# Optimization experiments

Measured on AMD Instinct MI355X. Metric: run time of the kernel, lower is better.

The kernel has to match this reference:

```python
import jax, jax.numpy as jnp
import numpy as np

B, L1, L2 = 4, 2048, 2048
INP1_DIM = INP2_DIM = 1024
QK_DIM = V_DIM = 1024
HEAD_N = 16
QK_HEAD = QK_DIM // HEAD_N  # 64
V_HEAD = V_DIM // HEAD_N    # 64
SCALE = 1.0 / (QK_HEAD ** 0.5)


def _linear_params(key, out_dim, in_dim):
    # torch nn.Linear default init: U(-1/sqrt(in), 1/sqrt(in)) for W and b
    kw, kb = jax.random.split(key)
    bound = 1.0 / np.sqrt(in_dim)
    W = jax.random.uniform(kw, (out_dim, in_dim), jnp.float32, -bound, bound)
    b = jax.random.uniform(kb, (out_dim,), jnp.float32, -bound, bound)
    return W, b


def setup_inputs() -> dict:
    key = jax.random.key(0)
    k1, k2, kq, kk, kv = jax.random.split(key, 5)
    inp1 = jax.random.normal(k1, (B, L1, INP1_DIM), jnp.float32)
    inp2 = jax.random.normal(k2, (B, L2, INP2_DIM), jnp.float32)
    Wq, bq = _linear_params(kq, QK_DIM, INP1_DIM)
    Wk, bk = _linear_params(kk, QK_DIM, INP2_DIM)
    Wv, bv = _linear_params(kv, V_DIM, INP2_DIM)
    return {"inp1": inp1, "inp2": inp2, "Wq": Wq, "bq": bq,
            "Wk": Wk, "bk": bk, "Wv": Wv, "bv": bv,
            "rescale_with_score": 1}


def reference(inp1, inp2, Wq, bq, Wk, bk, Wv, bv, rescale_with_score):
    b, l1, _ = inp1.shape
    l2 = inp2.shape[1]
    # torch Linear: x @ W.T + b
    q = (jnp.einsum('bld,ed->ble', inp1, Wq) + bq).reshape(b, l1, HEAD_N, QK_HEAD)
    k = (jnp.einsum('bmd,ed->bme', inp2, Wk) + bk).reshape(b, l2, HEAD_N, QK_HEAD)
    v = (jnp.einsum('bmd,ed->bme', inp2, Wv) + bv).reshape(b, l2, HEAD_N, V_HEAD)
    # scores: [b, l1, l2, h], softmax over l2 (axis=2)
    s = jax.nn.softmax(jnp.einsum('blhd,bmhd->blmh', q, k) * SCALE, axis=2)
    res = jnp.einsum('blmh,bmhd->blhd', s, v)  # [b, l1, h, v_head]
    if rescale_with_score:
        # per-query, per-head sum of squared attention weights -> [b, l1, h, 1]
        denom = jnp.sqrt(jnp.sum(s * s, axis=2))[..., None]
        res = res / denom
    return res.reshape(b, l1, -1)
```

## Files before the change

kernel.cpp:

```cpp
#include <hip/hip_runtime.h>
#include <hip/hip_bf16.h>

#define HEADS   16
#define HD      64
#define DMODEL  1024
#define LQ      2048
#define LK      2048
#define BATCH   4
#define MROWS   8192

typedef __attribute__((ext_vector_type(8))) short short8;
typedef __attribute__((ext_vector_type(4))) float f32x4;
typedef __attribute__((ext_vector_type(16))) float f32x16;
typedef __attribute__((ext_vector_type(2))) unsigned int uint2v;

union V4u { unsigned u[4]; short8 s8; };

static __device__ __forceinline__ unsigned short f2bf(float f) {
  unsigned u = __builtin_bit_cast(unsigned, f);
  u = (u + 0x7FFFu + ((u >> 16) & 1u)) >> 16;
  return (unsigned short)u;
}

static __device__ __forceinline__ unsigned cvtpk(float lo, float hi) {
  unsigned w;
  asm("v_cvt_pk_bf16_f32 %0, %1, %2" : "=v"(w) : "v"(lo), "v"(hi));
  return w;
}

static __device__ __forceinline__ void permswap(unsigned &a, unsigned &b) {
  asm volatile("v_permlane32_swap_b32 %0, %1" : "+v"(a), "+v"(b));
}

static __device__ __forceinline__ void gload_lds16(const void* g, void* l) {
  __builtin_amdgcn_global_load_lds(
      (const __attribute__((address_space(1))) unsigned int*)g,
      (__attribute__((address_space(3))) unsigned int*)l, 16, 0, 0);
}

static __device__ __forceinline__ unsigned lds_addr(const void* p) {
  return (unsigned)(size_t)(const __attribute__((address_space(3))) void*)p;
}

static __device__ __forceinline__ void ds_read128o(unsigned addr, int imm, V4u &d) {
  asm volatile("ds_read_b128 %0, %1 offset:%c2" : "=v"(d.s8) : "v"(addr), "i"(imm));
}

static __device__ __forceinline__ void ds_read_tro(unsigned addr, int imm, uint2v &d) {
  asm volatile("ds_read_b64_tr_b16 %0, %1 offset:%c2" : "=v"(d) : "v"(addr), "i"(imm));
}

__global__ void cvt_in_kernel(const float* __restrict__ s0, unsigned short* __restrict__ d0,
                              const float* __restrict__ s1, unsigned short* __restrict__ d1,
                              int n4) {
  int i = blockIdx.x * blockDim.x + threadIdx.x;
  if (i >= n4) return;
  const float* s = blockIdx.y ? s1 : s0;
  unsigned short* d = blockIdx.y ? d1 : d0;
  float4 v = ((const float4*)s)[i];
  ushort4 o;
  o.x = f2bf(v.x); o.y = f2bf(v.y); o.z = f2bf(v.z); o.w = f2bf(v.w);
  ((ushort4*)d)[i] = o;
}

__global__ void cvt_w_kernel(const float* __restrict__ s0, unsigned short* __restrict__ d0,
                             const float* __restrict__ s1, unsigned short* __restrict__ d1,
                             const float* __restrict__ s2, unsigned short* __restrict__ d2,
                             float scale0, int n4) {
  int i = blockIdx.x * blockDim.x + threadIdx.x;
  if (i >= n4) return;
  const float* s = blockIdx.y == 0 ? s0 : (blockIdx.y == 1 ? s1 : s2);
  unsigned short* d = blockIdx.y == 0 ? d0 : (blockIdx.y == 1 ? d1 : d2);
  float sc = blockIdx.y == 0 ? scale0 : 1.0f;
  float4 v = ((const float4*)s)[i];
  ushort4 o;
  o.x = f2bf(v.x * sc); o.y = f2bf(v.y * sc); o.z = f2bf(v.z * sc); o.w = f2bf(v.w * sc);
  ((ushort4*)d)[i] = o;
}

__global__ __launch_bounds__(256, 4) void gemm3_kernel(
    const unsigned short* __restrict__ X1,
    const unsigned short* __restrict__ X2,
    const unsigned short* __restrict__ Wqb,
    const unsigned short* __restrict__ Wkb,
    const unsigned short* __restrict__ Wvb,
    const float* __restrict__ bq,
    const float* __restrict__ bk,
    const float* __restrict__ bv,
    unsigned short* __restrict__ Qb,
    unsigned short* __restrict__ Kb,
    unsigned short* __restrict__ Vb,
    float cexp) {
  __shared__ __attribute__((aligned(16))) unsigned short As[128 * 32];
  __shared__ __attribute__((aligned(16))) unsigned short Bs[128 * 32];
  const int sel = blockIdx.z;
  const unsigned short* A = (sel == 0) ? X1 : X2;
  const unsigned short* W = (sel == 0) ? Wqb : (sel == 1) ? Wkb : Wvb;
  const float* bias = (sel == 0) ? bq : (sel == 1) ? bk : bv;
  unsigned short* C = (sel == 0) ? Qb : (sel == 1) ? Kb : Vb;
  const float bscale = (sel == 0) ? cexp : 1.0f;

  const int tid = threadIdx.x;
  const int l = tid & 63, w = tid >> 6;
  const int c = l & 15, g = l >> 4;
  const int wm = w >> 1, wn = w & 1;
  const int m0 = blockIdx.x * 128, n0 = blockIdx.y * 128;

  f32x4 acc[4][4];
#pragma unroll
  for (int i = 0; i < 4; ++i)
#pragma unroll
    for (int j = 0; j < 4; ++j) acc[i][j] = (f32x4){0.f, 0.f, 0.f, 0.f};

  for (int k0 = 0; k0 < 1024; k0 += 32) {
#pragma unroll
    for (int is = 0; is < 2; ++is) {
      int lin = is * 256 + tid;
      int r = lin >> 2, s = lin & 3;
      int gofs = (s ^ (r & 3)) * 8;
      gload_lds16(A + (size_t)(m0 + r) * 1024 + k0 + gofs,
                  &As[(is * 256 + (tid & ~63)) * 8]);
      gload_lds16(W + (size_t)(n0 + r) * 1024 + k0 + gofs,
                  &Bs[(is * 256 + (tid & ~63)) * 8]);
    }
    __syncthreads();
    short8 af[4], bfr[4];
#pragma unroll
    for (int mt = 0; mt < 4; ++mt) {
      int row = wm * 64 + mt * 16 + c;
      af[mt] = *(const short8*)((const char*)As + row * 64 + ((g ^ (row & 3)) << 4));
    }
#pragma unroll
    for (int nt = 0; nt < 4; ++nt) {
      int row = wn * 64 + nt * 16 + c;
      bfr[nt] = *(const short8*)((const char*)Bs + row * 64 + ((g ^ (row & 3)) << 4));
    }
    __builtin_amdgcn_s_setprio(1);
#pragma unroll
    for (int mt = 0; mt < 4; ++mt)
#pragma unroll
      for (int nt = 0; nt < 4; ++nt)
        acc[mt][nt] = __builtin_amdgcn_mfma_f32_16x16x32_bf16(af[mt], bfr[nt], acc[mt][nt], 0, 0, 0);
    __builtin_amdgcn_s_setprio(0);
    __syncthreads();
  }
  float bv4[4];
#pragma unroll
  for (int nt = 0; nt < 4; ++nt) bv4[nt] = bias[n0 + wn * 64 + nt * 16 + c] * bscale;
#pragma unroll
  for (int mt = 0; mt < 4; ++mt)
#pragma unroll
    for (int nt = 0; nt < 4; ++nt)
#pragma unroll
      for (int r = 0; r < 4; ++r) {
        int m = m0 + wm * 64 + mt * 16 + g * 4 + r;
        int n = n0 + wn * 64 + nt * 16 + c;
        C[(size_t)m * 1024 + n] = f2bf(acc[mt][nt][r] + bv4[nt]);
      }
}

__global__ __launch_bounds__(256) void attn_kernel(
    const unsigned short* __restrict__ Q,
    const unsigned short* __restrict__ K,
    const unsigned short* __restrict__ V,
    float* __restrict__ out,
    const int* __restrict__ rescale_flag) {
  __shared__ __attribute__((aligned(16))) unsigned short Kbuf[2][64 * 64];
  __shared__ __attribute__((aligned(16))) unsigned short Vbuf[2][64 * 64];
  __shared__ float ivLds[4][32];

  const int tid = threadIdx.x;
  const int lane = tid & 63, w = tid >> 6;
  const int l31 = lane & 31, hi = lane >> 5;

  const int gid = blockIdx.x;
  const int xcd = gid & 7;
  const int o = gid >> 3;
  const int bh = xcd * 8 + (o >> 4);
  const int qb = o & 15;
  const int bb = bh >> 4, h = bh & 15;
  const size_t qrowb = (size_t)bb * LQ + qb * 128 + w * 32;

  const int rs = *rescale_flag;

  short8 qf[4];
#pragma unroll
  for (int ks = 0; ks < 4; ++ks)
    qf[ks] = *(const short8*)(Q + (qrowb + l31) * 1024 + h * 64 + ks * 16 + hi * 8);

  const size_t kvbase = (size_t)bb * LK * 1024 + (size_t)h * 64;
  const int k_kv = tid >> 3;
  const int k_sl = (tid & 7) ^ (k_kv & 7);
  const unsigned short* ksrc0 = K + kvbase + (size_t)k_kv * 1024 + k_sl * 8;
  const unsigned short* ksrc1 = ksrc0 + (size_t)32 * 1024;
  const int v_kv = (w & 3) * 16 + ((lane >> 4) & 1) * 8 + ((lane >> 5) & 1) * 4 + ((lane >> 1) & 3);
  const int v_d  = ((lane >> 3) & 1) * 16 + (lane & 1) * 8;
  const unsigned short* vsrc0 = V + kvbase + (size_t)v_kv * 1024 + v_d;
  const unsigned short* vsrc1 = vsrc0 + 32;

  unsigned koff[4];
#pragma unroll
  for (int ks = 0; ks < 4; ++ks)
    koff[ks] = (unsigned)(l31 * 128 + ((((ks << 1) | hi) ^ (l31 & 7)) << 4));
  const unsigned kbase0 = lds_addr(&Kbuf[0][0]);
  const unsigned vbase0 = lds_addr(&Vbuf[0][0]);

  f32x16 po[2];
  po[0] = {}; po[1] = {};
  float zacc0 = 0.f, zacc1 = 0.f, s2acc0 = 0.f, s2acc1 = 0.f;

  gload_lds16(ksrc0, &Kbuf[0][w * 512]);
  gload_lds16(ksrc1, &Kbuf[0][(4 + w) * 512]);
  gload_lds16(vsrc0, &Vbuf[0][w * 512]);
  gload_lds16(vsrc1, &Vbuf[0][(4 + w) * 512]);
  __syncthreads();

  int cur = 0;
  for (int t = 0; t < LK / 64; ++t) {
    if (t < LK / 64 - 1) {
      const size_t adv = (size_t)(t + 1) * 65536;
      gload_lds16(ksrc0 + adv, &Kbuf[cur ^ 1][w * 512]);
      gload_lds16(ksrc1 + adv, &Kbuf[cur ^ 1][(4 + w) * 512]);
      gload_lds16(vsrc0 + adv, &Vbuf[cur ^ 1][w * 512]);
      gload_lds16(vsrc1 + adv, &Vbuf[cur ^ 1][(4 + w) * 512]);
    }
    unsigned kaddr[4];
#pragma unroll
    for (int ks = 0; ks < 4; ++ks) kaddr[ks] = kbase0 + (unsigned)(cur * 8192) + koff[ks];
    const unsigned vtr = vbase0 + (unsigned)(cur * 8192) + (unsigned)(lane * 8);

#pragma unroll
    for (int s = 0; s < 2; ++s) {
      V4u kfr[4];
#pragma unroll
      for (int ks = 0; ks < 4; ++ks) ds_read128o(kaddr[ks], s * 4096, kfr[ks]);
      uint2v ta0, ta1, ta2, ta3, tb0, tb1, tb2, tb3;
      ds_read_tro(vtr, (2 * s) * 1024, ta0);
      ds_read_tro(vtr, (2 * s) * 1024 + 512, ta1);
      ds_read_tro(vtr, (2 * s) * 1024 + 4096, ta2);
      ds_read_tro(vtr, (2 * s) * 1024 + 4608, ta3);
      ds_read_tro(vtr, (2 * s + 1) * 1024, tb0);
      ds_read_tro(vtr, (2 * s + 1) * 1024 + 512, tb1);
      ds_read_tro(vtr, (2 * s + 1) * 1024 + 4096, tb2);
      ds_read_tro(vtr, (2 * s + 1) * 1024 + 4608, tb3);
      asm volatile("s_waitcnt lgkmcnt(8)" ::: "memory");
      __builtin_amdgcn_sched_barrier(0);
      f32x16 ps = {};
      __builtin_amdgcn_s_setprio(1);
#pragma unroll
      for (int ks = 0; ks < 4; ++ks)
        ps = __builtin_amdgcn_mfma_f32_32x32x16_bf16(kfr[ks].s8, qf[ks], ps, 0, 0, 0);
      __builtin_amdgcn_s_setprio(0);
      float p[16];
#pragma unroll
      for (int r = 0; r < 16; ++r) p[r] = __builtin_amdgcn_exp2f(ps[r]);
      if (rs) {
#pragma unroll
        for (int r = 0; r < 8; ++r) {
          s2acc0 = fmaf(p[2 * r], p[2 * r], s2acc0);
          s2acc1 = fmaf(p[2 * r + 1], p[2 * r + 1], s2acc1);
        }
      } else {
#pragma unroll
        for (int r = 0; r < 8; ++r) {
          zacc0 += p[2 * r];
          zacc1 += p[2 * r + 1];
        }
      }
      unsigned wlo[4], whi[4];
#pragma unroll
      for (int b = 0; b < 4; ++b) {
        wlo[b] = cvtpk(p[4 * b + 0], p[4 * b + 1]);
        whi[b] = cvtpk(p[4 * b + 2], p[4 * b + 3]);
      }
      {
        unsigned a0 = wlo[0], b0 = wlo[1];
        unsigned a1 = whi[0], b1 = whi[1];
        permswap(a0, b0);
        permswap(a1, b1);
        V4u pau; pau.u[0] = a0; pau.u[1] = a1; pau.u[2] = b0; pau.u[3] = b1;
        asm volatile("s_waitcnt lgkmcnt(4)" ::: "memory");
        __builtin_amdgcn_sched_barrier(0);
        V4u v0u, v1u;
        v0u.u[0] = ta0[0]; v0u.u[1] = ta0[1]; v0u.u[2] = ta1[0]; v0u.u[3] = ta1[1];
        v1u.u[0] = ta2[0]; v1u.u[1] = ta2[1]; v1u.u[2] = ta3[0]; v1u.u[3] = ta3[1];
        __builtin_amdgcn_s_setprio(1);
        po[0] = __builtin_amdgcn_mfma_f32_32x32x16_bf16(pau.s8, v0u.s8, po[0], 0, 0, 0);
        po[1] = __builtin_amdgcn_mfma_f32_32x32x16_bf16(pau.s8, v1u.s8, po[1], 0, 0, 0);
        __builtin_amdgcn_s_setprio(0);
      }
      {
        unsigned a0 = wlo[2], b0 = wlo[3];
        unsigned a1 = whi[2], b1 = whi[3];
        permswap(a0, b0);
        permswap(a1, b1);
        V4u pau; pau.u[0] = a0; pau.u[1] = a1; pau.u[2] = b0; pau.u[3] = b1;
        asm volatile("s_waitcnt lgkmcnt(0)" ::: "memory");
        __builtin_amdgcn_sched_barrier(0);
        V4u v0u, v1u;
        v0u.u[0] = tb0[0]; v0u.u[1] = tb0[1]; v0u.u[2] = tb1[0]; v0u.u[3] = tb1[1];
        v1u.u[0] = tb2[0]; v1u.u[1] = tb2[1]; v1u.u[2] = tb3[0]; v1u.u[3] = tb3[1];
        __builtin_amdgcn_s_setprio(1);
        po[0] = __builtin_amdgcn_mfma_f32_32x32x16_bf16(pau.s8, v0u.s8, po[0], 0, 0, 0);
        po[1] = __builtin_amdgcn_mfma_f32_32x32x16_bf16(pau.s8, v1u.s8, po[1], 0, 0, 0);
        __builtin_amdgcn_s_setprio(0);
      }
    }
    __syncthreads();
    cur ^= 1;
  }

  float zacc = zacc0 + zacc1, s2acc = s2acc0 + s2acc1;
  float z2 = zacc + __shfl_xor(zacc, 32, 64);
  float s22 = s2acc + __shfl_xor(s2acc, 32, 64);
  float iv = rs ? (1.0f / sqrtf(s22)) : (1.0f / z2);
  ivLds[w][l31] = iv;

#pragma unroll
  for (int dt = 0; dt < 2; ++dt)
#pragma unroll
    for (int r = 0; r < 16; ++r) {
      const int ql = (r & 3) + 8 * (r >> 2) + 4 * hi;
      out[(qrowb + ql) * 1024 + h * 64 + dt * 32 + l31] = po[dt][r] * ivLds[w][ql];
    }
}

extern "C" void kernel_launch(void* const* d_in, const int* in_sizes, int n_in,
                              void* d_out, int out_size, void* d_ws, size_t ws_size,
                              hipStream_t stream) {
  const float* inp1 = (const float*)d_in[0];
  const float* inp2 = (const float*)d_in[1];
  const float* Wq = (const float*)d_in[2];
  const float* bq = (const float*)d_in[3];
  const float* Wk = (const float*)d_in[4];
  const float* bk = (const float*)d_in[5];
  const float* Wv = (const float*)d_in[6];
  const float* bv = (const float*)d_in[7];
  const int* rs = (const int*)d_in[8];
  float* out = (float*)d_out;

  const float CEXP = 0.18033688011112042f;

  unsigned short* X1  = (unsigned short*)d_ws;
  unsigned short* X2  = X1 + (size_t)MROWS * 1024;
  unsigned short* Wqb = X2 + (size_t)MROWS * 1024;
  unsigned short* Wkb = Wqb + (size_t)1024 * 1024;
  unsigned short* Wvb = Wkb + (size_t)1024 * 1024;
  unsigned short* Qb  = Wvb + (size_t)1024 * 1024;
  unsigned short* Kb  = Qb + (size_t)MROWS * 1024;
  unsigned short* Vb  = Kb + (size_t)MROWS * 1024;

  cvt_in_kernel<<<dim3(MROWS * 1024 / 1024, 2), 256, 0, stream>>>(inp1, X1, inp2, X2, MROWS * 1024 / 4);
  cvt_w_kernel<<<dim3(1024, 3), 256, 0, stream>>>(Wq, Wqb, Wk, Wkb, Wv, Wvb, CEXP, 1024 * 1024 / 4);

  gemm3_kernel<<<dim3(64, 8, 3), 256, 0, stream>>>(X1, X2, Wqb, Wkb, Wvb,
                                                   bq, bk, bv, Qb, Kb, Vb, CEXP);

  attn_kernel<<<dim3(1024), 256, 0, stream>>>(Qb, Kb, Vb, out, rs);
}
```

Measured before the change: 174.7 us.

## Double attention block to 8 waves sharing K/V tiles, split QK MFMA chains

```diff
diff --git a/kernel.cpp b/kernel.cpp
--- a/kernel.cpp
+++ b/kernel.cpp
@@ -12,9 +12,11 @@
 typedef __attribute__((ext_vector_type(8))) short short8;
 typedef __attribute__((ext_vector_type(4))) float f32x4;
 typedef __attribute__((ext_vector_type(16))) float f32x16;
+typedef __attribute__((ext_vector_type(2))) float f32x2;
 typedef __attribute__((ext_vector_type(2))) unsigned int uint2v;
 
 union V4u { unsigned u[4]; short8 s8; };
+union PSu { f32x16 v; f32x2 pr[8]; };
 
 static __device__ __forceinline__ unsigned short f2bf(float f) {
   unsigned u = __builtin_bit_cast(unsigned, f);
@@ -30,6 +32,16 @@
 
 static __device__ __forceinline__ void permswap(unsigned &a, unsigned &b) {
   asm volatile("v_permlane32_swap_b32 %0, %1" : "+v"(a), "+v"(b));
+}
+
+static __device__ __forceinline__ void pk_add(f32x2 &d, f32x2 a, f32x2 b) {
+  asm("v_pk_add_f32 %0, %1, %2" : "=v"(d) : "v"(a), "v"(b));
+}
+static __device__ __forceinline__ void pk_add_acc(f32x2 &acc, f32x2 p) {
+  asm("v_pk_add_f32 %0, %1, %0" : "+v"(acc) : "v"(p));
+}
+static __device__ __forceinline__ void pk_fma_acc(f32x2 &acc, f32x2 p) {
+  asm("v_pk_fma_f32 %0, %1, %1, %0" : "+v"(acc) : "v"(p));
 }
 
 static __device__ __forceinline__ void gload_lds16(const void* g, void* l) {
@@ -159,7 +171,7 @@
       }
 }
 
-__global__ __launch_bounds__(256) void attn_kernel(
+__global__ __launch_bounds__(512) void attn_kernel(
     const unsigned short* __restrict__ Q,
     const unsigned short* __restrict__ K,
     const unsigned short* __restrict__ V,
@@ -167,7 +179,7 @@
     const int* __restrict__ rescale_flag) {
   __shared__ __attribute__((aligned(16))) unsigned short Kbuf[2][64 * 64];
   __shared__ __attribute__((aligned(16))) unsigned short Vbuf[2][64 * 64];
-  __shared__ float ivLds[4][32];
+  __shared__ float ivLds[8][32];
 
   const int tid = threadIdx.x;
   const int lane = tid & 63, w = tid >> 6;
@@ -176,10 +188,10 @@
   const int gid = blockIdx.x;
   const int xcd = gid & 7;
   const int o = gid >> 3;
-  const int bh = xcd * 8 + (o >> 4);
-  const int qb = o & 15;
+  const int bh = xcd * 8 + (o >> 3);
+  const int qb = o & 7;
   const int bb = bh >> 4, h = bh & 15;
-  const size_t qrowb = (size_t)bb * LQ + qb * 128 + w * 32;
+  const size_t qrowb = (size_t)bb * LQ + qb * 256 + w * 32;
 
   const int rs = *rescale_flag;
 
@@ -189,14 +201,12 @@
     qf[ks] = *(const short8*)(Q + (qrowb + l31) * 1024 + h * 64 + ks * 16 + hi * 8);
 
   const size_t kvbase = (size_t)bb * LK * 1024 + (size_t)h * 64;
-  const int k_kv = tid >> 3;
-  const int k_sl = (tid & 7) ^ (k_kv & 7);
+  const int k_kv = w * 8 + (lane >> 3);
+  const int k_sl = (lane & 7) ^ (lane >> 3);
   const unsigned short* ksrc0 = K + kvbase + (size_t)k_kv * 1024 + k_sl * 8;
-  const unsigned short* ksrc1 = ksrc0 + (size_t)32 * 1024;
   const int v_kv = (w & 3) * 16 + ((lane >> 4) & 1) * 8 + ((lane >> 5) & 1) * 4 + ((lane >> 1) & 3);
-  const int v_d  = ((lane >> 3) & 1) * 16 + (lane & 1) * 8;
+  const int v_d  = (w >> 2) * 32 + ((lane >> 3) & 1) * 16 + (lane & 1) * 8;
   const unsigned short* vsrc0 = V + kvbase + (size_t)v_kv * 1024 + v_d;
-  const unsigned short* vsrc1 = vsrc0 + 32;
 
   unsigned koff[4];
 #pragma unroll
@@ -207,22 +217,19 @@
 
   f32x16 po[2];
   po[0] = {}; po[1] = {};
-  float zacc0 = 0.f, zacc1 = 0.f, s2acc0 = 0.f, s2acc1 = 0.f;
+  f32x2 za[2], s2a[2];
+  za[0] = (f32x2){0.f, 0.f}; za[1] = (f32x2){0.f, 0.f};
+  s2a[0] = (f32x2){0.f, 0.f}; s2a[1] = (f32x2){0.f, 0.f};
 
   gload_lds16(ksrc0, &Kbuf[0][w * 512]);
-  gload_lds16(ksrc1, &Kbuf[0][(4 + w) * 512]);
   gload_lds16(vsrc0, &Vbuf[0][w * 512]);
-  gload_lds16(vsrc1, &Vbuf[0][(4 + w) * 512]);
   __syncthreads();
 
   int cur = 0;
   for (int t = 0; t < LK / 64; ++t) {
     if (t < LK / 64 - 1) {
-      const size_t adv = (size_t)(t + 1) * 65536;
-      gload_lds16(ksrc0 + adv, &Kbuf[cur ^ 1][w * 512]);
-      gload_lds16(ksrc1 + adv, &Kbuf[cur ^ 1][(4 + w) * 512]);
-      gload_lds16(vsrc0 + adv, &Vbuf[cur ^ 1][w * 512]);
-      gload_lds16(vsrc1 + adv, &Vbuf[cur ^ 1][(4 + w) * 512]);
+      gload_lds16(ksrc0 + (size_t)(t + 1) * 65536, &Kbuf[cur ^ 1][w * 512]);
+      gload_lds16(vsrc0 + (size_t)(t + 1) * 65536, &Vbuf[cur ^ 1][w * 512]);
     }
     unsigned kaddr[4];
 #pragma unroll
@@ -245,33 +252,35 @@
       ds_read_tro(vtr, (2 * s + 1) * 1024 + 4608, tb3);
       asm volatile("s_waitcnt lgkmcnt(8)" ::: "memory");
       __builtin_amdgcn_sched_barrier(0);
-      f32x16 ps = {};
+      PSu ps0u, ps1u;
+      ps0u.v = (f32x16){};
+      ps1u.v = (f32x16){};
       __builtin_amdgcn_s_setprio(1);
-#pragma unroll
-      for (int ks = 0; ks < 4; ++ks)
-        ps = __builtin_amdgcn_mfma_f32_32x32x16_bf16(kfr[ks].s8, qf[ks], ps, 0, 0, 0);
+      ps0u.v = __builtin_amdgcn_mfma_f32_32x32x16_bf16(kfr[0].s8, qf[0], ps0u.v, 0, 0, 0);
+      ps1u.v = __builtin_amdgcn_mfma_f32_32x32x16_bf16(kfr[1].s8, qf[1], ps1u.v, 0, 0, 0);
+      ps0u.v = __builtin_amdgcn_mfma_f32_32x32x16_bf16(kfr[2].s8, qf[2], ps0u.v, 0, 0, 0);
+      ps1u.v = __builtin_amdgcn_mfma_f32_32x32x16_bf16(kfr[3].s8, qf[3], ps1u.v, 0, 0, 0);
       __builtin_amdgcn_s_setprio(0);
-      float p[16];
-#pragma unroll
-      for (int r = 0; r < 16; ++r) p[r] = __builtin_amdgcn_exp2f(ps[r]);
+      f32x2 p2[8];
+#pragma unroll
+      for (int b = 0; b < 8; ++b) {
+        f32x2 tmerge;
+        pk_add(tmerge, ps0u.pr[b], ps1u.pr[b]);
+        p2[b].x = __builtin_amdgcn_exp2f(tmerge.x);
+        p2[b].y = __builtin_amdgcn_exp2f(tmerge.y);
+      }
       if (rs) {
 #pragma unroll
-        for (int r = 0; r < 8; ++r) {
-          s2acc0 = fmaf(p[2 * r], p[2 * r], s2acc0);
-          s2acc1 = fmaf(p[2 * r + 1], p[2 * r + 1], s2acc1);
-        }
+        for (int b = 0; b < 8; ++b) pk_fma_acc(s2a[b & 1], p2[b]);
       } else {
 #pragma unroll
-        for (int r = 0; r < 8; ++r) {
-          zacc0 += p[2 * r];
-          zacc1 += p[2 * r + 1];
-        }
+        for (int b = 0; b < 8; ++b) pk_add_acc(za[b & 1], p2[b]);
       }
       unsigned wlo[4], whi[4];
 #pragma unroll
       for (int b = 0; b < 4; ++b) {
-        wlo[b] = cvtpk(p[4 * b + 0], p[4 * b + 1]);
-        whi[b] = cvtpk(p[4 * b + 2], p[4 * b + 3]);
+        wlo[b] = cvtpk(p2[2 * b].x, p2[2 * b].y);
+        whi[b] = cvtpk(p2[2 * b + 1].x, p2[2 * b + 1].y);
       }
       {
         unsigned a0 = wlo[0], b0 = wlo[1];
@@ -310,7 +319,8 @@
     cur ^= 1;
   }
 
-  float zacc = zacc0 + zacc1, s2acc = s2acc0 + s2acc1;
+  float zacc = za[0].x + za[0].y + za[1].x + za[1].y;
+  float s2acc = s2a[0].x + s2a[0].y + s2a[1].x + s2a[1].y;
   float z2 = zacc + __shfl_xor(zacc, 32, 64);
   float s22 = s2acc + __shfl_xor(s2acc, 32, 64);
   float iv = rs ? (1.0f / sqrtf(s22)) : (1.0f / z2);
@@ -356,5 +366,5 @@
   gemm3_kernel<<<dim3(64, 8, 3), 256, 0, stream>>>(X1, X2, Wqb, Wkb, Wvb,
                                                    bq, bk, bv, Qb, Kb, Vb, CEXP);
 
-  attn_kernel<<<dim3(1024), 256, 0, stream>>>(Qb, Kb, Vb, out, rs);
-}
+  attn_kernel<<<dim3(512), 512, 0, stream>>>(Qb, Kb, Vb, out, rs);
+}
```

Result: faster. 169.3 us (-3.1%).
